# Performance work log

Measured on AMD Instinct MI355X. Metric: run time of the kernel, lower is better.

Reference implementation:

```python
import jax, jax.numpy as jnp
import numpy as np

B, P, D, VP, VD = 256, 1152, 10, 8, 16
NUM_ITER = 3


def setup_inputs() -> dict:
    key = jax.random.key(0)
    k1, k2 = jax.random.split(key)
    x = jax.random.normal(k1, (B, P, VP, 1), dtype=jnp.float32)
    # learned transform matrices, init randn/100 as in the torch module
    W = jax.random.normal(k2, (P, D, VD, VP), dtype=jnp.float32) / 100.0
    return {"x": x, "W": W}


def _squash(s, axis):
    # v = ||s||^2/(1+||s||^2) * s/||s||
    sq = jnp.sum(s * s, axis=axis, keepdims=True)
    return s * sq / (1.0 + sq) / jnp.sqrt(sq + 1e-9)


def reference(x, W):
    xs = x[..., 0]                                      # [B,P,8]
    # u_hat[b,p,d,:] = W[p,d] @ x[b,p]  (no explicit stack/broadcast materialization)
    u_hat = jnp.einsum('pdij,bpj->bpdi', W, xs)          # [B,P,D,16]
    u_stop = jax.lax.stop_gradient(u_hat)
    b_ij = jnp.zeros((B, P, D, 1), dtype=u_hat.dtype)    # torch b_ij [B,P,D,1,1], trailing 1 dropped
    v = None
    for it in range(NUM_ITER):
        # faithful to source: softmax over torch dim=3 (size-1 axis) -> all ones
        c_ij = jax.nn.softmax(b_ij, axis=3)               # [B,P,D,1]
        u = u_hat if it == NUM_ITER - 1 else u_stop
        s_j = jnp.sum(c_ij * u, axis=1)                   # [B,D,16]
        v = _squash(s_j, axis=2)                          # [B,D,16]
        if it != NUM_ITER - 1:
            # agreement: u_hat^T v -> scalar per (b,p,d)
            upd = jnp.einsum('bpdi,bdi->bpd', u_hat, v)[..., None]
            b_ij = b_ij + upd
    return v[..., None]                                   # [B,D,16,1] matching torch output
```

## Files before the change

### kernel.cpp

```cpp
#include <hip/hip_runtime.h>
#include <math.h>

#define M 256
#define N 160
#define K 9216
#define CH 72
#define KC 128
#define BM 64

using f32x4 = __attribute__((ext_vector_type(4))) float;
using bf16x8 = __attribute__((ext_vector_type(8))) short;

__device__ __forceinline__ ushort f2bf(float f) {
  uint u = __builtin_bit_cast(uint, f);
  u += 0x7FFF + ((u >> 16) & 1);
  return (ushort)(u >> 16);
}

template <bool ATOMIC>
__global__ __launch_bounds__(256) void gemm_mfma(const float* __restrict__ x,
                                                 const float* __restrict__ W,
                                                 float* __restrict__ part) {
  __shared__ ushort Xl[BM * KC];
  __shared__ ushort Wl[N * KC];

  const int t = threadIdx.x;
  const int mt = blockIdx.x & 3;
  const int c = blockIdx.x >> 2;
  const int m0 = mt * BM;
  const int k0 = c * KC;

  {
    const float* xs = x + (size_t)m0 * K + k0;
#pragma unroll
    for (int q = 0; q < 8; ++q) {
      const int f = t + 256 * q;
      const int row = f >> 5;
      const int kq = (f & 31) << 2;
      const float4 v = *(const float4*)(xs + (size_t)row * K + kq);
      ushort4 h = {f2bf(v.x), f2bf(v.y), f2bf(v.z), f2bf(v.w)};
      const int E = (row * KC + kq) ^ ((row & 7) << 3);
      *(ushort4*)&Xl[E] = h;
    }
  }
  {
    const float* ws = W + (size_t)(c * 16) * 1280;
#pragma unroll
    for (int q = 0; q < 20; ++q) {
      const int f = t + 256 * q;
      const float4 v = *(const float4*)(ws + 4 * (size_t)f);
      const int pl = f / 320;
      const int r = f - pl * 320;
      const int d = r >> 5;
      const int idx = r & 31;
      const int i = idx >> 1;
      const int j = (idx & 1) << 2;
      const int n = d * 16 + i;
      const int kk = pl * 8 + j;
      ushort4 h = {f2bf(v.x), f2bf(v.y), f2bf(v.z), f2bf(v.w)};
      const int E = (n * KC + kk) ^ ((n & 7) << 3);
      *(ushort4*)&Wl[E] = h;
    }
  }
  __syncthreads();

  const int w = t >> 6;
  const int l = t & 63;
  const int lr = l & 15;
  const int lg = l >> 4;

  f32x4 acc[10];
#pragma unroll
  for (int nt = 0; nt < 10; ++nt) acc[nt] = {0.f, 0.f, 0.f, 0.f};

#pragma unroll
  for (int ks = 0; ks < 4; ++ks) {
    const int arow = w * 16 + lr;
    const int EA = (arow * KC + ks * 32 + lg * 8) ^ ((arow & 7) << 3);
    const bf16x8 a = *(const bf16x8*)&Xl[EA];
#pragma unroll
    for (int nt = 0; nt < 10; ++nt) {
      const int n = nt * 16 + lr;
      const int EB = (n * KC + ks * 32 + lg * 8) ^ ((n & 7) << 3);
      const bf16x8 b = *(const bf16x8*)&Wl[EB];
      acc[nt] =
          __builtin_amdgcn_mfma_f32_16x16x32_bf16(a, b, acc[nt], 0, 0, 0);
    }
  }

  if (ATOMIC) {
#pragma unroll
    for (int nt = 0; nt < 10; ++nt)
#pragma unroll
      for (int r = 0; r < 4; ++r) {
        const int row = m0 + w * 16 + lg * 4 + r;
        atomicAdd(&part[(size_t)row * N + nt * 16 + lr], acc[nt][r]);
      }
  } else {
    float* dst = part + (size_t)c * (M * N);
#pragma unroll
    for (int nt = 0; nt < 10; ++nt)
#pragma unroll
      for (int r = 0; r < 4; ++r) {
        const int row = m0 + w * 16 + lg * 4 + r;
        dst[(size_t)row * N + nt * 16 + lr] = acc[nt][r];
      }
  }
}

__global__ __launch_bounds__(256) void reduce_squash(
    const float* __restrict__ part, float* __restrict__ out) {
  __shared__ float red[256];
  const int t = threadIdx.x;
  const int base = blockIdx.x * 64;
  const int o = t & 63;
  const int slice = t >> 6;
  float sum = 0.f;
#pragma unroll 6
  for (int cc = 0; cc < 18; ++cc) {
    const int c = slice * 18 + cc;
    sum += part[(size_t)c * (M * N) + base + o];
  }
  red[t] = sum;
  __syncthreads();
  if (t < 64) {
    const float s = red[t] + red[t + 64] + red[t + 128] + red[t + 192];
    float s2 = s * s;
    s2 += __shfl_xor(s2, 1);
    s2 += __shfl_xor(s2, 2);
    s2 += __shfl_xor(s2, 4);
    s2 += __shfl_xor(s2, 8);
    out[base + t] = s * s2 / (1.0f + s2) / sqrtf(s2 + 1e-9f);
  }
}

__global__ __launch_bounds__(256) void squash_k(float* __restrict__ out) {
  const int e = blockIdx.x * 256 + threadIdx.x;
  const float s = out[e];
  float s2 = s * s;
  s2 += __shfl_xor(s2, 1);
  s2 += __shfl_xor(s2, 2);
  s2 += __shfl_xor(s2, 4);
  s2 += __shfl_xor(s2, 8);
  out[e] = s * s2 / (1.0f + s2) / sqrtf(s2 + 1e-9f);
}

extern "C" void kernel_launch(void* const* d_in, const int* in_sizes, int n_in,
                              void* d_out, int out_size, void* d_ws,
                              size_t ws_size, hipStream_t stream) {
  const float* x = (const float*)d_in[0];
  const float* W = (const float*)d_in[1];
  float* out = (float*)d_out;

  const size_t need = (size_t)CH * M * N * sizeof(float);
  if (ws_size >= need) {
    gemm_mfma<false><<<4 * CH, 256, 0, stream>>>(x, W, (float*)d_ws);
    reduce_squash<<<(M * N) / 64, 256, 0, stream>>>((const float*)d_ws, out);
  } else {
    hipMemsetAsync(out, 0, (size_t)M * N * sizeof(float), stream);
    gemm_mfma<true><<<4 * CH, 256, 0, stream>>>(x, W, out);
    squash_k<<<(M * N) / 256, 256, 0, stream>>>(out);
  }
}
```

Baseline: 18.16 us.

## Load A fragments directly to registers, remap blocks per XCD, vectorize reduction

The GEMM kernel now loads each lane's x fragment straight from global memory into registers and converts it to bf16 there, removing the X shared-memory tile and its LDS round trip. Blocks are remapped so that the four M-tiles sharing a K-chunk of W are scheduled on the same XCD, which should improve L2 reuse of W. The reduce+squash kernel processes float4 per thread, using a quarter as many blocks with vectorized loads and a two-step shuffle for the 16-element norm. The per-lane x loads are 32-byte strided row reads and are less coalesced than the old cooperative tile load.

```diff
diff --git a/kernel.cpp b/kernel.cpp
--- a/kernel.cpp
+++ b/kernel.cpp
@@ -21,28 +21,30 @@
 __global__ __launch_bounds__(256) void gemm_mfma(const float* __restrict__ x,
                                                  const float* __restrict__ W,
                                                  float* __restrict__ part) {
-  __shared__ ushort Xl[BM * KC];
   __shared__ ushort Wl[N * KC];
 
   const int t = threadIdx.x;
-  const int mt = blockIdx.x & 3;
-  const int c = blockIdx.x >> 2;
+  const int bx = blockIdx.x;
+  const int xcd = bx & 7;
+  const int idx = bx >> 3;
+  const int c = xcd * 9 + (idx >> 2);
+  const int mt = idx & 3;
   const int m0 = mt * BM;
   const int k0 = c * KC;
 
-  {
-    const float* xs = x + (size_t)m0 * K + k0;
+  const int w = t >> 6;
+  const int l = t & 63;
+  const int lr = l & 15;
+  const int lg = l >> 4;
+
+  const float* xr = x + (size_t)(m0 + w * 16 + lr) * K + k0;
+  float4 araw[4][2];
 #pragma unroll
-    for (int q = 0; q < 8; ++q) {
-      const int f = t + 256 * q;
-      const int row = f >> 5;
-      const int kq = (f & 31) << 2;
-      const float4 v = *(const float4*)(xs + (size_t)row * K + kq);
-      ushort4 h = {f2bf(v.x), f2bf(v.y), f2bf(v.z), f2bf(v.w)};
-      const int E = (row * KC + kq) ^ ((row & 7) << 3);
-      *(ushort4*)&Xl[E] = h;
-    }
+  for (int ks = 0; ks < 4; ++ks) {
+    araw[ks][0] = *(const float4*)(xr + ks * 32 + lg * 8);
+    araw[ks][1] = *(const float4*)(xr + ks * 32 + lg * 8 + 4);
   }
+
   {
     const float* ws = W + (size_t)(c * 16) * 1280;
 #pragma unroll
@@ -52,9 +54,9 @@
       const int pl = f / 320;
       const int r = f - pl * 320;
       const int d = r >> 5;
-      const int idx = r & 31;
-      const int i = idx >> 1;
-      const int j = (idx & 1) << 2;
+      const int idx2 = r & 31;
+      const int i = idx2 >> 1;
+      const int j = (idx2 & 1) << 2;
       const int n = d * 16 + i;
       const int kk = pl * 8 + j;
       ushort4 h = {f2bf(v.x), f2bf(v.y), f2bf(v.z), f2bf(v.w)};
@@ -62,12 +64,20 @@
       *(ushort4*)&Wl[E] = h;
     }
   }
+
+  bf16x8 af[4];
+#pragma unroll
+  for (int ks = 0; ks < 4; ++ks) {
+    af[ks][0] = (short)f2bf(araw[ks][0].x);
+    af[ks][1] = (short)f2bf(araw[ks][0].y);
+    af[ks][2] = (short)f2bf(araw[ks][0].z);
+    af[ks][3] = (short)f2bf(araw[ks][0].w);
+    af[ks][4] = (short)f2bf(araw[ks][1].x);
+    af[ks][5] = (short)f2bf(araw[ks][1].y);
+    af[ks][6] = (short)f2bf(araw[ks][1].z);
+    af[ks][7] = (short)f2bf(araw[ks][1].w);
+  }
   __syncthreads();
-
-  const int w = t >> 6;
-  const int l = t & 63;
-  const int lr = l & 15;
-  const int lg = l >> 4;
 
   f32x4 acc[10];
 #pragma unroll
@@ -75,16 +85,13 @@
 
 #pragma unroll
   for (int ks = 0; ks < 4; ++ks) {
-    const int arow = w * 16 + lr;
-    const int EA = (arow * KC + ks * 32 + lg * 8) ^ ((arow & 7) << 3);
-    const bf16x8 a = *(const bf16x8*)&Xl[EA];
 #pragma unroll
     for (int nt = 0; nt < 10; ++nt) {
       const int n = nt * 16 + lr;
       const int EB = (n * KC + ks * 32 + lg * 8) ^ ((n & 7) << 3);
       const bf16x8 b = *(const bf16x8*)&Wl[EB];
       acc[nt] =
-          __builtin_amdgcn_mfma_f32_16x16x32_bf16(a, b, acc[nt], 0, 0, 0);
+          __builtin_amdgcn_mfma_f32_16x16x32_bf16(af[ks], b, acc[nt], 0, 0, 0);
     }
   }
 
@@ -108,29 +115,31 @@
   }
 }
 
-__global__ __launch_bounds__(256) void reduce_squash(
+__global__ __launch_bounds__(256) void reduce_squash4(
     const float* __restrict__ part, float* __restrict__ out) {
-  __shared__ float red[256];
+  __shared__ f32x4 red[256];
   const int t = threadIdx.x;
-  const int base = blockIdx.x * 64;
-  const int o = t & 63;
+  const int o4 = t & 63;
   const int slice = t >> 6;
-  float sum = 0.f;
+  const f32x4* p4 = (const f32x4*)part;
+  const int base4 = blockIdx.x * 64;
+
+  f32x4 sum = {0.f, 0.f, 0.f, 0.f};
 #pragma unroll 6
   for (int cc = 0; cc < 18; ++cc) {
     const int c = slice * 18 + cc;
-    sum += part[(size_t)c * (M * N) + base + o];
+    sum += p4[(size_t)c * (M * N / 4) + base4 + o4];
   }
   red[t] = sum;
   __syncthreads();
   if (t < 64) {
-    const float s = red[t] + red[t + 64] + red[t + 128] + red[t + 192];
-    float s2 = s * s;
-    s2 += __shfl_xor(s2, 1);
-    s2 += __shfl_xor(s2, 2);
-    s2 += __shfl_xor(s2, 4);
-    s2 += __shfl_xor(s2, 8);
-    out[base + t] = s * s2 / (1.0f + s2) / sqrtf(s2 + 1e-9f);
+    const f32x4 s = red[t] + red[t + 64] + red[t + 128] + red[t + 192];
+    float n2 = s[0] * s[0] + s[1] * s[1] + s[2] * s[2] + s[3] * s[3];
+    n2 += __shfl_xor(n2, 1);
+    n2 += __shfl_xor(n2, 2);
+    const float sc = n2 / (1.0f + n2) / sqrtf(n2 + 1e-9f);
+    f32x4 o = {s[0] * sc, s[1] * sc, s[2] * sc, s[3] * sc};
+    ((f32x4*)out)[base4 + t] = o;
   }
 }
 
@@ -155,7 +164,7 @@
   const size_t need = (size_t)CH * M * N * sizeof(float);
   if (ws_size >= need) {
     gemm_mfma<false><<<4 * CH, 256, 0, stream>>>(x, W, (float*)d_ws);
-    reduce_squash<<<(M * N) / 64, 256, 0, stream>>>((const float*)d_ws, out);
+    reduce_squash4<<<(M * N) / 256, 256, 0, stream>>>((const float*)d_ws, out);
   } else {
     hipMemsetAsync(out, 0, (size_t)M * N * sizeof(float), stream);
     gemm_mfma<true><<<4 * CH, 256, 0, stream>>>(x, W, out);
```

New measurement: 19.45 us. +7.1%, slower.
